# Optimization experiments

Hardware: AMD Instinct MI355X
Metric: run time of the kernel (lower is better)

## Reference

```python
import jax, jax.numpy as jnp
import numpy as np

D_MODEL = 1024
N_HEADS = 16
SEQ = 4096
BATCH = 1
THETA = 10000.0


def setup_inputs() -> dict:
    key = jax.random.key(0)
    ks = jax.random.split(key, 5)
    std = np.sqrt(2.0 / (D_MODEL + D_MODEL))
    x = jax.random.normal(ks[0], (BATCH, SEQ, D_MODEL), dtype=jnp.float32)
    Wq = jax.random.normal(ks[1], (D_MODEL, D_MODEL), dtype=jnp.float32) * std
    Wk = jax.random.normal(ks[2], (D_MODEL, D_MODEL), dtype=jnp.float32) * std
    Wv = jax.random.normal(ks[3], (D_MODEL, D_MODEL), dtype=jnp.float32) * std
    Wo = jax.random.normal(ks[4], (D_MODEL, D_MODEL), dtype=jnp.float32) * std
    token_positions = jnp.arange(SEQ, dtype=jnp.int32)
    return {"x": x, "Wq": Wq, "Wk": Wk, "Wv": Wv, "Wo": Wo,
            "token_positions": token_positions}


def _rope(x, positions):
    # x: [b, h, s, d]; positions: [s]
    d = x.shape[-1]
    ks = jnp.arange(0, d, 2, dtype=jnp.float32)
    inv_freq = 1.0 / jnp.power(jnp.float32(THETA), ks / d)          # [d/2]
    ang = positions.astype(jnp.float32)[:, None] * inv_freq[None, :]  # [s, d/2]
    cos, sin = jnp.cos(ang), jnp.sin(ang)
    x_even, x_odd = x[..., 0::2], x[..., 1::2]
    y_even = cos * x_even - sin * x_odd
    y_odd = sin * x_even + cos * x_odd
    # interleave back: [..., d/2, 2] -> [..., d]
    return jnp.stack([y_even, y_odd], axis=-1).reshape(x.shape)


def reference(x, Wq, Wk, Wv, Wo, token_positions):
    b, s, _ = x.shape
    h = N_HEADS
    d = D_MODEL // h

    def proj(W):
        y = jnp.einsum('bsi,oi->bso', x, W)
        return y.reshape(b, s, h, d).transpose(0, 2, 1, 3)  # [b,h,s,d]

    Q, K, V = proj(Wq), proj(Wk), proj(Wv)
    Q = _rope(Q, token_positions)
    K = _rope(K, token_positions)

    scale = 1.0 / np.sqrt(d)
    scores = jnp.einsum('bhqd,bhkd->bhqk', Q, K) * scale  # [b,h,s,s]
    causal = jnp.tril(jnp.ones((s, s), dtype=bool))
    scores = jnp.where(causal, scores, -jnp.inf)
    attn = jax.nn.softmax(scores, axis=-1)
    ctx = jnp.einsum('bhqk,bhkd->bhqd', attn, V)
    ctx = ctx.transpose(0, 2, 1, 3).reshape(b, s, D_MODEL)
    return jnp.einsum('bsi,oi->bso', ctx, Wo)
```

## Files before the change

### kernel.cpp

```cpp
#include <hip/hip_runtime.h>
#include <hip/hip_bf16.h>
#include <stdint.h>

#define S_LEN 4096
#define D_MODEL 1024
#define N_HEADS 16
#define D_HEAD 64
#define SCALE_LOG2E 0.1803368787f

typedef __attribute__((ext_vector_type(4))) float f32x4;
typedef __attribute__((ext_vector_type(8))) __bf16 bf16x8;
typedef __attribute__((ext_vector_type(4))) __bf16 bf16x4;

__device__ __forceinline__ unsigned short f2bf(float f) {
    union { float f; unsigned u; } x{f};
    unsigned r = x.u + 0x7fff + ((x.u >> 16) & 1);
    return (unsigned short)(r >> 16);
}

__device__ __forceinline__ void gld_lds16(const void* g, void* l) {
    __builtin_amdgcn_global_load_lds(
        (const __attribute__((address_space(1))) unsigned int*)g,
        (__attribute__((address_space(3))) unsigned int*)l, 16, 0, 0);
}

__global__ __launch_bounds__(256) void to_bf16_k(const float* __restrict__ src,
                                                 unsigned short* __restrict__ dst, int n) {
    int i = (blockIdx.x * 256 + threadIdx.x) * 4;
    if (i < n) {
        float4 v = *(const float4*)&src[i];
        ushort4 o;
        o.x = f2bf(v.x); o.y = f2bf(v.y); o.z = f2bf(v.z); o.w = f2bf(v.w);
        *(ushort4*)&dst[i] = o;
    }
}

__global__ __launch_bounds__(256) void wconv_k(const float* __restrict__ a,
                                               const float* __restrict__ b,
                                               const float* __restrict__ c,
                                               const float* __restrict__ d,
                                               unsigned short* __restrict__ dst) {
    int i = (blockIdx.x * 256 + threadIdx.x) * 4;
    int sel = i >> 20;
    int off = i & ((1 << 20) - 1);
    const float* src = (sel == 0) ? a : (sel == 1) ? b : (sel == 2) ? c : d;
    float4 v = *(const float4*)&src[off];
    ushort4 o;
    o.x = f2bf(v.x); o.y = f2bf(v.y); o.z = f2bf(v.z); o.w = f2bf(v.w);
    *(ushort4*)&dst[i] = o;
}

__global__ __launch_bounds__(256) void rope_tables_k(const int* __restrict__ pos,
                                                     float* __restrict__ ct,
                                                     float* __restrict__ st) {
    int i = blockIdx.x * 256 + threadIdx.x;
    int s = i >> 5, k = i & 31;
    float invf = __builtin_exp2f(-(float)(2 * k) * (1.0f / 64.0f) * 13.287712379549449f);
    float ang = (float)pos[s] * invf;
    ct[i] = cosf(ang);
    st[i] = sinf(ang);
}

__global__ __launch_bounds__(256) void vtrans_k(const unsigned short* __restrict__ src,
                                                unsigned short* __restrict__ dst) {
    __shared__ unsigned short tile[64 * 68];
    const int bs = blockIdx.x * 64;
    const int bd = blockIdx.y * 64;
    const int t = threadIdx.x;
    {
        int col = (t & 7) * 8;
        #pragma unroll
        for (int rr = 0; rr < 2; ++rr) {
            int row = rr * 32 + (t >> 3);
            const unsigned short* g = src + (size_t)(bs + row) * D_MODEL + bd + col;
            ushort4 a = *(const ushort4*)g;
            ushort4 b = *(const ushort4*)(g + 4);
            *(ushort4*)&tile[row * 68 + col] = a;
            *(ushort4*)&tile[row * 68 + col + 4] = b;
        }
    }
    __syncthreads();
    {
        int dl = t >> 2;
        int sc = (t & 3) * 16;
        ushort4 o[4];
        #pragma unroll
        for (int e = 0; e < 16; ++e)
            ((unsigned short*)o)[e] = tile[(sc + e) * 68 + dl];
        unsigned short* g = dst + (size_t)(bd + dl) * S_LEN + bs + sc;
        *(ushort4*)(g + 0)  = o[0];
        *(ushort4*)(g + 4)  = o[1];
        *(ushort4*)(g + 8)  = o[2];
        *(ushort4*)(g + 12) = o[3];
    }
}

template <int MODE>
__global__ __launch_bounds__(256) void gemm_nt_k(const unsigned short* __restrict__ A,
                                                 const unsigned short* __restrict__ B,
                                                 void* __restrict__ Cout,
                                                 int M, int N, int K,
                                                 const float* __restrict__ costab,
                                                 const float* __restrict__ sintab,
                                                 float scl) {
    __shared__ unsigned short lA[128 * 64];
    __shared__ unsigned short lB[128 * 64];
    const int t = threadIdx.x, w = t >> 6, l = t & 63;
    const int tm = blockIdx.y * 128, tn = blockIdx.x * 128;
    const int wm = (w >> 1) * 64, wn = (w & 1) * 64;
    const int g = l >> 4, ln = l & 15;

    f32x4 acc[4][4] = {};

    for (int k0 = 0; k0 < K; k0 += 64) {
        #pragma unroll
        for (int r = 0; r < 4; ++r) {
            int row = 8 * (4 * r + w) + (l >> 3);
            const unsigned short* ga = A + (size_t)(tm + row) * K + k0 + (l & 7) * 8;
            gld_lds16(ga, &lA[(4 * r + w) * 512]);
            const unsigned short* gb = B + (size_t)(tn + row) * K + k0 + (l & 7) * 8;
            gld_lds16(gb, &lB[(4 * r + w) * 512]);
        }
        asm volatile("s_waitcnt vmcnt(0)" ::: "memory");
        __syncthreads();

        #pragma unroll
        for (int kk = 0; kk < 2; ++kk) {
            bf16x8 af[4], bf[4];
            #pragma unroll
            for (int i = 0; i < 4; ++i) {
                af[i] = *(const bf16x8*)&lA[(wm + i * 16 + ln) * 64 + kk * 32 + g * 8];
                bf[i] = *(const bf16x8*)&lB[(wn + i * 16 + ln) * 64 + kk * 32 + g * 8];
            }
            #pragma unroll
            for (int i = 0; i < 4; ++i)
                #pragma unroll
                for (int j = 0; j < 4; ++j)
                    acc[i][j] = __builtin_amdgcn_mfma_f32_16x16x32_bf16(af[i], bf[j], acc[i][j], 0, 0, 0);
        }
        __syncthreads();
    }

    #pragma unroll
    for (int i = 0; i < 4; ++i) {
        #pragma unroll
        for (int j = 0; j < 4; ++j) {
            int col = tn + wn + j * 16 + ln;
            #pragma unroll
            for (int r = 0; r < 4; ++r) {
                int row = tm + wm + i * 16 + g * 4 + r;
                float v = acc[i][j][r];
                if (MODE == 1) {
                    float p = __shfl_xor(v, 1, 64);
                    int dd = col & 63;
                    int kidx = dd >> 1;
                    float c = costab[row * 32 + kidx];
                    float s = sintab[row * 32 + kidx];
                    v = ((dd & 1) ? (s * p + c * v) : (c * v - s * p)) * scl;
                }
                if (MODE == 2)
                    ((float*)Cout)[(size_t)row * N + col] = v;
                else
                    ((unsigned short*)Cout)[(size_t)row * N + col] = f2bf(v);
            }
        }
    }
}

__device__ __forceinline__ void stage8(const unsigned short* __restrict__ Kb,
                                       const unsigned short* __restrict__ Vt,
                                       unsigned short* lK, unsigned short* lV,
                                       int h, int kt, int w, int l) {
    const int half = w & 3;
    const int chunk = (l & 7) ^ (l >> 3);
    if (w < 4) {
        #pragma unroll
        for (int r2 = 0; r2 < 2; ++r2) {
            int row = half * 16 + r2 * 8 + (l >> 3);
            gld_lds16(Kb + (size_t)(kt * 64 + row) * D_MODEL + h * 64 + chunk * 8,
                      lK + half * 1024 + r2 * 512);
        }
    } else {
        #pragma unroll
        for (int r2 = 0; r2 < 2; ++r2) {
            int row = half * 16 + r2 * 8 + (l >> 3);
            gld_lds16(Vt + (size_t)(h * 64 + row) * S_LEN + kt * 64 + chunk * 8,
                      lV + half * 1024 + r2 * 512);
        }
    }
}

__global__ __launch_bounds__(512) void attn_k(const unsigned short* __restrict__ Qb,
                                              const unsigned short* __restrict__ Kb,
                                              const unsigned short* __restrict__ Vt,
                                              unsigned short* __restrict__ ctxb) {
    __shared__ unsigned short lK[2][64 * 64];
    __shared__ unsigned short lV[2][64 * 64];
    __shared__ unsigned short lP[8][16 * 64];

    const int t = threadIdx.x, w = t >> 6, l = t & 63;
    const int wv = w & 3;
    const int sel = w >> 2;
    const int h = blockIdx.x;
    const int qA = blockIdx.y;
    const int qB = 63 - qA;
    const int qT = sel ? qB : qA;
    const int q0 = qT * 64 + wv * 16;
    const int g = l >> 4, ln = l & 15;

    bf16x8 aq[2];
    #pragma unroll
    for (int kk = 0; kk < 2; ++kk)
        aq[kk] = *(const bf16x8*)&Qb[(size_t)(q0 + ln) * D_MODEL + h * 64 + kk * 32 + g * 8];

    f32x4 acc[4] = {};
    float rm = -INFINITY, rs = 0.0f;
    char* lpw = (char*)&lP[w][0];

    stage8(Kb, Vt, &lK[0][0], &lV[0][0], h, 0, w, l);
    asm volatile("s_waitcnt vmcnt(0)" ::: "memory");
    __syncthreads();

    int cur = 0;
    for (int kt = 0; kt <= qB; ++kt) {
        if (kt < qB)
            stage8(Kb, Vt, &lK[cur ^ 1][0], &lV[cur ^ 1][0], h, kt + 1, w, l);

        if (kt <= qT) {
            float p[16];
            __builtin_amdgcn_s_setprio(1);
            #pragma unroll
            for (int ct = 0; ct < 4; ++ct) {
                f32x4 z = {};
                #pragma unroll
                for (int kk = 0; kk < 2; ++kk) {
                    int row = ct * 16 + ln;
                    int off = (row * 128 + kk * 64 + g * 16) ^ ((row & 7) << 4);
                    bf16x8 ak = *(const bf16x8*)((const char*)&lK[cur][0] + off);
                    z = __builtin_amdgcn_mfma_f32_16x16x32_bf16(ak, aq[kk], z, 0, 0, 0);
                }
                #pragma unroll
                for (int r = 0; r < 4; ++r) p[ct * 4 + r] = z[r];
            }
            __builtin_amdgcn_s_setprio(0);

            if (kt == qT) {
                int qg = q0 + ln;
                #pragma unroll
                for (int ct = 0; ct < 4; ++ct)
                    #pragma unroll
                    for (int r = 0; r < 4; ++r)
                        if (kt * 64 + ct * 16 + g * 4 + r > qg) p[ct * 4 + r] = -INFINITY;
            }

            float pmax = fmaxf(p[0], p[1]);
            #pragma unroll
            for (int i = 2; i < 16; i += 2)
                pmax = fmaxf(fmaxf(pmax, p[i]), p[i + 1]);
            pmax = fmaxf(pmax, __shfl_xor(pmax, 16, 64));
            pmax = fmaxf(pmax, __shfl_xor(pmax, 32, 64));
            if (__any(pmax > rm + 8.0f)) {
                float mn = fmaxf(rm, pmax);
                float fac = __builtin_amdgcn_exp2f(rm - mn);
                rm = mn;
                rs *= fac;
                #pragma unroll
                for (int mb = 0; mb < 4; ++mb) {
                    f32x4 a = acc[mb];
                    #pragma unroll
                    for (int r = 0; r < 4; ++r) a[r] *= fac;
                    acc[mb] = a;
                }
            }
            float ps = 0.0f;
            #pragma unroll
            for (int i = 0; i < 16; ++i) {
                float e = __builtin_amdgcn_exp2f(p[i] - rm);
                p[i] = e;
                ps += e;
            }
            ps += __shfl_xor(ps, 16, 64);
            ps += __shfl_xor(ps, 32, 64);
            rs += ps;

            #pragma unroll
            for (int ct = 0; ct < 4; ++ct) {
                bf16x4 pv;
                pv[0] = (__bf16)p[ct * 4 + 0];
                pv[1] = (__bf16)p[ct * 4 + 1];
                pv[2] = (__bf16)p[ct * 4 + 2];
                pv[3] = (__bf16)p[ct * 4 + 3];
                int off = (ln * 128 + ct * 32 + g * 8) ^ ((ln & 7) << 4);
                *(bf16x4*)(lpw + off) = pv;
            }

            __builtin_amdgcn_s_setprio(1);
            #pragma unroll
            for (int mb = 0; mb < 4; ++mb) {
                #pragma unroll
                for (int kc = 0; kc < 2; ++kc) {
                    int vrow = mb * 16 + ln;
                    int voff = (vrow * 128 + kc * 64 + g * 16) ^ ((vrow & 7) << 4);
                    bf16x8 av = *(const bf16x8*)((const char*)&lV[cur][0] + voff);
                    int poff = (ln * 128 + kc * 64 + g * 16) ^ ((ln & 7) << 4);
                    bf16x8 bp = *(const bf16x8*)(lpw + poff);
                    acc[mb] = __builtin_amdgcn_mfma_f32_16x16x32_bf16(av, bp, acc[mb], 0, 0, 0);
                }
            }
            __builtin_amdgcn_s_setprio(0);
        }

        asm volatile("s_waitcnt vmcnt(0)" ::: "memory");
        __syncthreads();
        cur ^= 1;
    }

    float inv = 1.0f / rs;
    #pragma unroll
    for (int mb = 0; mb < 4; ++mb) {
        bf16x4 o;
        #pragma unroll
        for (int r = 0; r < 4; ++r) o[r] = (__bf16)(acc[mb][r] * inv);
        *(bf16x4*)&ctxb[(size_t)(q0 + ln) * D_MODEL + h * 64 + mb * 16 + g * 4] = o;
    }
}

extern "C" void kernel_launch(void* const* d_in, const int* in_sizes, int n_in,
                              void* d_out, int out_size, void* d_ws, size_t ws_size,
                              hipStream_t stream) {
    const float* x  = (const float*)d_in[0];
    const float* Wq = (const float*)d_in[1];
    const float* Wk = (const float*)d_in[2];
    const float* Wv = (const float*)d_in[3];
    const float* Wo = (const float*)d_in[4];
    const int* tpos = (const int*)d_in[5];
    float* out = (float*)d_out;

    char* ws = (char*)d_ws;
    unsigned short* xb   = (unsigned short*)(ws + 0);
    unsigned short* Wqb  = (unsigned short*)(ws + (8u << 20));
    unsigned short* Wkb  = (unsigned short*)(ws + (10u << 20));
    unsigned short* Wvb  = (unsigned short*)(ws + (12u << 20));
    unsigned short* Wob  = (unsigned short*)(ws + (14u << 20));
    unsigned short* Qbuf = (unsigned short*)(ws + (16u << 20));
    unsigned short* Kbuf = (unsigned short*)(ws + (24u << 20));
    unsigned short* Vtb  = (unsigned short*)(ws + (32u << 20));
    unsigned short* ctxb = (unsigned short*)(ws + (40u << 20));
    unsigned short* Vrow = ctxb;
    float* costab = (float*)(ws + (48u << 20));
    float* sintab = (float*)(ws + (48u << 20) + (512u << 10));

    to_bf16_k<<<4096, 256, 0, stream>>>(x, xb, S_LEN * D_MODEL);
    wconv_k<<<4096, 256, 0, stream>>>(Wq, Wk, Wv, Wo, Wqb);
    rope_tables_k<<<512, 256, 0, stream>>>(tpos, costab, sintab);

    dim3 gg(D_MODEL / 128, S_LEN / 128);
    gemm_nt_k<1><<<gg, 256, 0, stream>>>(xb, Wqb, Qbuf, S_LEN, D_MODEL, D_MODEL,
                                         costab, sintab, SCALE_LOG2E);
    gemm_nt_k<1><<<gg, 256, 0, stream>>>(xb, Wkb, Kbuf, S_LEN, D_MODEL, D_MODEL,
                                         costab, sintab, 1.0f);
    gemm_nt_k<0><<<gg, 256, 0, stream>>>(xb, Wvb, Vrow, S_LEN, D_MODEL, D_MODEL,
                                         nullptr, nullptr, 1.0f);
    vtrans_k<<<dim3(S_LEN / 64, D_MODEL / 64), 256, 0, stream>>>(Vrow, Vtb);

    attn_k<<<dim3(N_HEADS, 32), 512, 0, stream>>>(Qbuf, Kbuf, Vtb, ctxb);

    gemm_nt_k<2><<<gg, 256, 0, stream>>>(ctxb, Wob, out, S_LEN, D_MODEL, D_MODEL,
                                         nullptr, nullptr, 1.0f);
}
```

Baseline: 199.0 us.

## Fuse QKV projections into one GEMM, merge prep kernels, retile output GEMM

Merges the three conversion and rope-table kernels into a single prep launch. Replaces the three separate Q/K/V GEMMs with one 3072-wide GEMM that writes an interleaved QKV buffer. Rope and scale are applied per column range, with identity rows in the table for the V columns. The output projection gets a 64x128 tile kernel so more blocks run per launch. The goal is to cut launch overhead and fill more CUs, at the cost of strided QKV accesses in the attention and transpose kernels.

```diff
diff --git a/kernel.cpp b/kernel.cpp
--- a/kernel.cpp
+++ b/kernel.cpp
@@ -6,6 +6,7 @@
 #define D_MODEL 1024
 #define N_HEADS 16
 #define D_HEAD 64
+#define LDQKV 3072
 #define SCALE_LOG2E 0.1803368787f
 
 typedef __attribute__((ext_vector_type(4))) float f32x4;
@@ -24,41 +25,45 @@
         (__attribute__((address_space(3))) unsigned int*)l, 16, 0, 0);
 }
 
-__global__ __launch_bounds__(256) void to_bf16_k(const float* __restrict__ src,
-                                                 unsigned short* __restrict__ dst, int n) {
-    int i = (blockIdx.x * 256 + threadIdx.x) * 4;
-    if (i < n) {
-        float4 v = *(const float4*)&src[i];
+__global__ __launch_bounds__(256) void prep_k(const float* __restrict__ x,
+                                              const float* __restrict__ Wq,
+                                              const float* __restrict__ Wk,
+                                              const float* __restrict__ Wv,
+                                              const float* __restrict__ Wo,
+                                              const int* __restrict__ pos,
+                                              unsigned short* __restrict__ xb,
+                                              unsigned short* __restrict__ Wb,
+                                              float* __restrict__ ct,
+                                              float* __restrict__ st) {
+    int b = blockIdx.x;
+    if (b < 4096) {
+        int i = (b * 256 + threadIdx.x) * 4;
+        float4 v = *(const float4*)&x[i];
         ushort4 o;
         o.x = f2bf(v.x); o.y = f2bf(v.y); o.z = f2bf(v.z); o.w = f2bf(v.w);
-        *(ushort4*)&dst[i] = o;
-    }
-}
-
-__global__ __launch_bounds__(256) void wconv_k(const float* __restrict__ a,
-                                               const float* __restrict__ b,
-                                               const float* __restrict__ c,
-                                               const float* __restrict__ d,
-                                               unsigned short* __restrict__ dst) {
-    int i = (blockIdx.x * 256 + threadIdx.x) * 4;
-    int sel = i >> 20;
-    int off = i & ((1 << 20) - 1);
-    const float* src = (sel == 0) ? a : (sel == 1) ? b : (sel == 2) ? c : d;
-    float4 v = *(const float4*)&src[off];
-    ushort4 o;
-    o.x = f2bf(v.x); o.y = f2bf(v.y); o.z = f2bf(v.z); o.w = f2bf(v.w);
-    *(ushort4*)&dst[i] = o;
-}
-
-__global__ __launch_bounds__(256) void rope_tables_k(const int* __restrict__ pos,
-                                                     float* __restrict__ ct,
-                                                     float* __restrict__ st) {
-    int i = blockIdx.x * 256 + threadIdx.x;
-    int s = i >> 5, k = i & 31;
-    float invf = __builtin_exp2f(-(float)(2 * k) * (1.0f / 64.0f) * 13.287712379549449f);
-    float ang = (float)pos[s] * invf;
-    ct[i] = cosf(ang);
-    st[i] = sinf(ang);
+        *(ushort4*)&xb[i] = o;
+    } else if (b < 8192) {
+        int i = ((b - 4096) * 256 + threadIdx.x) * 4;
+        int sel = i >> 20;
+        int off = i & ((1 << 20) - 1);
+        const float* src = (sel == 0) ? Wq : (sel == 1) ? Wk : (sel == 2) ? Wv : Wo;
+        float4 v = *(const float4*)&src[off];
+        ushort4 o;
+        o.x = f2bf(v.x); o.y = f2bf(v.y); o.z = f2bf(v.z); o.w = f2bf(v.w);
+        *(ushort4*)&Wb[i] = o;
+    } else {
+        int i = (b - 8192) * 256 + threadIdx.x;
+        int s = i >> 6, k = i & 63;
+        if (k < 32) {
+            float invf = __builtin_exp2f(-(float)(2 * k) * (1.0f / 64.0f) * 13.287712379549449f);
+            float ang = (float)pos[s] * invf;
+            ct[i] = cosf(ang);
+            st[i] = sinf(ang);
+        } else {
+            ct[i] = 1.0f;
+            st[i] = 0.0f;
+        }
+    }
 }
 
 __global__ __launch_bounds__(256) void vtrans_k(const unsigned short* __restrict__ src,
@@ -72,7 +77,7 @@
         #pragma unroll
         for (int rr = 0; rr < 2; ++rr) {
             int row = rr * 32 + (t >> 3);
-            const unsigned short* g = src + (size_t)(bs + row) * D_MODEL + bd + col;
+            const unsigned short* g = src + (size_t)(bs + row) * LDQKV + bd + col;
             ushort4 a = *(const ushort4*)g;
             ushort4 b = *(const ushort4*)(g + 4);
             *(ushort4*)&tile[row * 68 + col] = a;
@@ -95,14 +100,11 @@
     }
 }
 
-template <int MODE>
-__global__ __launch_bounds__(256) void gemm_nt_k(const unsigned short* __restrict__ A,
-                                                 const unsigned short* __restrict__ B,
-                                                 void* __restrict__ Cout,
-                                                 int M, int N, int K,
-                                                 const float* __restrict__ costab,
-                                                 const float* __restrict__ sintab,
-                                                 float scl) {
+__global__ __launch_bounds__(256) void gemm_qkv_k(const unsigned short* __restrict__ A,
+                                                  const unsigned short* __restrict__ B,
+                                                  unsigned short* __restrict__ C,
+                                                  const float* __restrict__ ct,
+                                                  const float* __restrict__ st) {
     __shared__ unsigned short lA[128 * 64];
     __shared__ unsigned short lB[128 * 64];
     const int t = threadIdx.x, w = t >> 6, l = t & 63;
@@ -112,14 +114,12 @@
 
     f32x4 acc[4][4] = {};
 
-    for (int k0 = 0; k0 < K; k0 += 64) {
+    for (int k0 = 0; k0 < 1024; k0 += 64) {
         #pragma unroll
         for (int r = 0; r < 4; ++r) {
             int row = 8 * (4 * r + w) + (l >> 3);
-            const unsigned short* ga = A + (size_t)(tm + row) * K + k0 + (l & 7) * 8;
-            gld_lds16(ga, &lA[(4 * r + w) * 512]);
-            const unsigned short* gb = B + (size_t)(tn + row) * K + k0 + (l & 7) * 8;
-            gld_lds16(gb, &lB[(4 * r + w) * 512]);
+            gld_lds16(A + (size_t)(tm + row) * 1024 + k0 + (l & 7) * 8, &lA[(4 * r + w) * 512]);
+            gld_lds16(B + (size_t)(tn + row) * 1024 + k0 + (l & 7) * 8, &lB[(4 * r + w) * 512]);
         }
         asm volatile("s_waitcnt vmcnt(0)" ::: "memory");
         __syncthreads();
@@ -146,25 +146,78 @@
         #pragma unroll
         for (int j = 0; j < 4; ++j) {
             int col = tn + wn + j * 16 + ln;
+            int dd = col & 63;
+            int tb = ((col >= 2048) ? 32 : 0) + (dd >> 1);
+            float scl = (col < 1024) ? SCALE_LOG2E : 1.0f;
             #pragma unroll
             for (int r = 0; r < 4; ++r) {
                 int row = tm + wm + i * 16 + g * 4 + r;
                 float v = acc[i][j][r];
-                if (MODE == 1) {
-                    float p = __shfl_xor(v, 1, 64);
-                    int dd = col & 63;
-                    int kidx = dd >> 1;
-                    float c = costab[row * 32 + kidx];
-                    float s = sintab[row * 32 + kidx];
-                    v = ((dd & 1) ? (s * p + c * v) : (c * v - s * p)) * scl;
-                }
-                if (MODE == 2)
-                    ((float*)Cout)[(size_t)row * N + col] = v;
-                else
-                    ((unsigned short*)Cout)[(size_t)row * N + col] = f2bf(v);
-            }
-        }
-    }
+                float p = __shfl_xor(v, 1, 64);
+                float c = ct[row * 64 + tb];
+                float s = st[row * 64 + tb];
+                v = ((dd & 1) ? (s * p + c * v) : (c * v - s * p)) * scl;
+                C[(size_t)row * LDQKV + col] = f2bf(v);
+            }
+        }
+    }
+}
+
+__global__ __launch_bounds__(256) void gemm_o_k(const unsigned short* __restrict__ A,
+                                                const unsigned short* __restrict__ B,
+                                                float* __restrict__ C) {
+    __shared__ unsigned short lA[64 * 64];
+    __shared__ unsigned short lB[128 * 64];
+    const int t = threadIdx.x, w = t >> 6, l = t & 63;
+    const int tm = blockIdx.y * 64, tn = blockIdx.x * 128;
+    const int wm = (w >> 1) * 32, wn = (w & 1) * 64;
+    const int g = l >> 4, ln = l & 15;
+
+    f32x4 acc[2][4] = {};
+
+    for (int k0 = 0; k0 < 1024; k0 += 64) {
+        #pragma unroll
+        for (int r = 0; r < 2; ++r) {
+            int row = r * 32 + w * 8 + (l >> 3);
+            gld_lds16(A + (size_t)(tm + row) * 1024 + k0 + (l & 7) * 8, &lA[(r * 32 + w * 8) * 64]);
+        }
+        #pragma unroll
+        for (int r = 0; r < 4; ++r) {
+            int row = 8 * (4 * r + w) + (l >> 3);
+            gld_lds16(B + (size_t)(tn + row) * 1024 + k0 + (l & 7) * 8, &lB[(4 * r + w) * 512]);
+        }
+        asm volatile("s_waitcnt vmcnt(0)" ::: "memory");
+        __syncthreads();
+
+        #pragma unroll
+        for (int kk = 0; kk < 2; ++kk) {
+            bf16x8 af[2], bf[4];
+            #pragma unroll
+            for (int i = 0; i < 2; ++i)
+                af[i] = *(const bf16x8*)&lA[(wm + i * 16 + ln) * 64 + kk * 32 + g * 8];
+            #pragma unroll
+            for (int j = 0; j < 4; ++j)
+                bf[j] = *(const bf16x8*)&lB[(wn + j * 16 + ln) * 64 + kk * 32 + g * 8];
+            #pragma unroll
+            for (int i = 0; i < 2; ++i)
+                #pragma unroll
+                for (int j = 0; j < 4; ++j)
+                    acc[i][j] = __builtin_amdgcn_mfma_f32_16x16x32_bf16(af[i], bf[j], acc[i][j], 0, 0, 0);
+        }
+        __syncthreads();
+    }
+
+    #pragma unroll
+    for (int i = 0; i < 2; ++i)
+        #pragma unroll
+        for (int j = 0; j < 4; ++j) {
+            int col = tn + wn + j * 16 + ln;
+            #pragma unroll
+            for (int r = 0; r < 4; ++r) {
+                int row = tm + wm + i * 16 + g * 4 + r;
+                C[(size_t)row * 1024 + col] = acc[i][j][r];
+            }
+        }
 }
 
 __device__ __forceinline__ void stage8(const unsigned short* __restrict__ Kb,
@@ -177,7 +230,7 @@
         #pragma unroll
         for (int r2 = 0; r2 < 2; ++r2) {
             int row = half * 16 + r2 * 8 + (l >> 3);
-            gld_lds16(Kb + (size_t)(kt * 64 + row) * D_MODEL + h * 64 + chunk * 8,
+            gld_lds16(Kb + (size_t)(kt * 64 + row) * LDQKV + h * 64 + chunk * 8,
                       lK + half * 1024 + r2 * 512);
         }
     } else {
@@ -211,7 +264,7 @@
     bf16x8 aq[2];
     #pragma unroll
     for (int kk = 0; kk < 2; ++kk)
-        aq[kk] = *(const bf16x8*)&Qb[(size_t)(q0 + ln) * D_MODEL + h * 64 + kk * 32 + g * 8];
+        aq[kk] = *(const bf16x8*)&Qb[(size_t)(q0 + ln) * LDQKV + h * 64 + kk * 32 + g * 8];
 
     f32x4 acc[4] = {};
     float rm = -INFINITY, rs = 0.0f;
@@ -338,33 +391,20 @@
 
     char* ws = (char*)d_ws;
     unsigned short* xb   = (unsigned short*)(ws + 0);
-    unsigned short* Wqb  = (unsigned short*)(ws + (8u << 20));
-    unsigned short* Wkb  = (unsigned short*)(ws + (10u << 20));
-    unsigned short* Wvb  = (unsigned short*)(ws + (12u << 20));
-    unsigned short* Wob  = (unsigned short*)(ws + (14u << 20));
-    unsigned short* Qbuf = (unsigned short*)(ws + (16u << 20));
-    unsigned short* Kbuf = (unsigned short*)(ws + (24u << 20));
-    unsigned short* Vtb  = (unsigned short*)(ws + (32u << 20));
+    unsigned short* Wb   = (unsigned short*)(ws + (8u << 20));
+    unsigned short* QKV  = (unsigned short*)(ws + (16u << 20));
     unsigned short* ctxb = (unsigned short*)(ws + (40u << 20));
-    unsigned short* Vrow = ctxb;
     float* costab = (float*)(ws + (48u << 20));
-    float* sintab = (float*)(ws + (48u << 20) + (512u << 10));
-
-    to_bf16_k<<<4096, 256, 0, stream>>>(x, xb, S_LEN * D_MODEL);
-    wconv_k<<<4096, 256, 0, stream>>>(Wq, Wk, Wv, Wo, Wqb);
-    rope_tables_k<<<512, 256, 0, stream>>>(tpos, costab, sintab);
-
-    dim3 gg(D_MODEL / 128, S_LEN / 128);
-    gemm_nt_k<1><<<gg, 256, 0, stream>>>(xb, Wqb, Qbuf, S_LEN, D_MODEL, D_MODEL,
-                                         costab, sintab, SCALE_LOG2E);
-    gemm_nt_k<1><<<gg, 256, 0, stream>>>(xb, Wkb, Kbuf, S_LEN, D_MODEL, D_MODEL,
-                                         costab, sintab, 1.0f);
-    gemm_nt_k<0><<<gg, 256, 0, stream>>>(xb, Wvb, Vrow, S_LEN, D_MODEL, D_MODEL,
-                                         nullptr, nullptr, 1.0f);
-    vtrans_k<<<dim3(S_LEN / 64, D_MODEL / 64), 256, 0, stream>>>(Vrow, Vtb);
-
-    attn_k<<<dim3(N_HEADS, 32), 512, 0, stream>>>(Qbuf, Kbuf, Vtb, ctxb);
-
-    gemm_nt_k<2><<<gg, 256, 0, stream>>>(ctxb, Wob, out, S_LEN, D_MODEL, D_MODEL,
-                                         nullptr, nullptr, 1.0f);
-}
+    float* sintab = (float*)(ws + (49u << 20));
+    unsigned short* Vtb  = xb;
+
+    prep_k<<<9216, 256, 0, stream>>>(x, Wq, Wk, Wv, Wo, tpos, xb, Wb, costab, sintab);
+
+    gemm_qkv_k<<<dim3(24, 32), 256, 0, stream>>>(xb, Wb, QKV, costab, sintab);
+
+    vtrans_k<<<dim3(S_LEN / 64, D_MODEL / 64), 256, 0, stream>>>(QKV + 2048, Vtb);
+
+    attn_k<<<dim3(N_HEADS, 32), 512, 0, stream>>>(QKV, QKV + 1024, Vtb, ctxb);
+
+    gemm_o_k<<<dim3(8, 64), 256, 0, stream>>>(ctxb, Wb + 3u * 1024 * 1024, out);
+}
```

Result: faster. 165.2 us (median of 3 runs) (-17.0%).
